# Kernel optimization log

Measured on AMD Instinct MI355X. Metric: run time of the kernel, lower is better.

Reference implementation:

```python
import jax, jax.numpy as jnp
import numpy as np
from jax import lax

B, CIN, COUT, H, W = 4, 256, 256, 64, 64
KH = KW = 3
STRIDE = PAD = DIL = 1
GROUPS = 1
K = KH * KW
HO = (H + 2 * PAD - DIL * (KH - 1) - 1) // STRIDE + 1
WO = (W + 2 * PAD - DIL * (KW - 1) - 1) // STRIDE + 1
DN = ('NCHW', 'OIHW', 'NCHW')


def _sep_conv(x, dw, pw):
    # Separable2d: depthwise kxk conv (stride/pad/dilation) then pointwise 1x1.
    y = lax.conv_general_dilated(x, dw, (STRIDE, STRIDE), [(PAD, PAD), (PAD, PAD)],
                                 rhs_dilation=(DIL, DIL), feature_group_count=x.shape[1],
                                 dimension_numbers=DN)
    return lax.conv_general_dilated(y, pw, (1, 1), 'VALID', dimension_numbers=DN)


def _deform_conv2d(x, offset, mask, weight, bias):
    Bb, Cin, Hh, Ww = x.shape
    O = weight.shape[0]
    G = offset.shape[1] // (2 * K)  # offset groups
    offs = offset.reshape(Bb, G, K, 2, HO, WO)
    dy, dx = offs[:, :, :, 0], offs[:, :, :, 1]  # [B,G,K,Ho,Wo]
    ki, kj = jnp.meshgrid(jnp.arange(KH), jnp.arange(KW), indexing='ij')
    base_y = (-PAD + ki.reshape(K, 1) * DIL + jnp.arange(HO)[None, :] * STRIDE).astype(x.dtype)  # [K,Ho]
    base_x = (-PAD + kj.reshape(K, 1) * DIL + jnp.arange(WO)[None, :] * STRIDE).astype(x.dtype)  # [K,Wo]
    py = base_y[None, None, :, :, None] + dy  # [B,G,K,Ho,Wo]
    px = base_x[None, None, :, None, :] + dx

    xg = x.reshape(Bb, G, Cin // G, Hh, Ww)

    def bilinear(img, py, px):
        # img [C,H,W], py/px [K,Ho,Wo]; zero-padding outside bounds.
        y0 = jnp.floor(py)
        x0 = jnp.floor(px)
        out = jnp.zeros((img.shape[0],) + py.shape, img.dtype)
        for a, (iy, wy) in enumerate((((y0), (y0 + 1 - py)), ((y0 + 1), (py - y0)))):
            for b, (ix, wx) in enumerate((((x0), (x0 + 1 - px)), ((x0 + 1), (px - x0)))):
                valid = (iy >= 0) & (iy < Hh) & (ix >= 0) & (ix < Ww)
                iyc = jnp.clip(iy, 0, Hh - 1).astype(jnp.int32)
                ixc = jnp.clip(ix, 0, Ww - 1).astype(jnp.int32)
                v = img[:, iyc, ixc]  # [C,K,Ho,Wo]
                out = out + v * (wy * wx * valid)[None]
        return out

    sampled = jax.vmap(jax.vmap(bilinear))(xg, py, px)  # [B,G,C/G,K,Ho,Wo]
    m = mask.reshape(Bb, G, K, HO, WO)
    sampled = sampled * m[:, :, None]

    cols = sampled.reshape(Bb, Cin, K, HO, WO).reshape(Bb, GROUPS, Cin // GROUPS, K, HO, WO)
    wr = weight.reshape(GROUPS, O // GROUPS, Cin // GROUPS, K)
    out = jnp.einsum('bgckhw,gock->bgohw', cols, wr).reshape(Bb, O, HO, WO)
    return out + bias[None, :, None, None]


def setup_inputs() -> dict:
    key = jax.random.key(0)
    ks = jax.random.split(key, 7)
    x = jax.random.normal(ks[0], (B, CIN, H, W), jnp.float32)
    weight = jax.random.normal(ks[1], (COUT, CIN // GROUPS, KH, KW), jnp.float32) / np.sqrt(CIN * K)
    bias = jax.random.normal(ks[2], (COUT,), jnp.float32) * 0.01
    off_dw = jax.random.normal(ks[3], (CIN, 1, KH, KW), jnp.float32) * 0.01
    off_pw = jax.random.normal(ks[4], (2 * K * GROUPS, CIN, 1, 1), jnp.float32) * 0.01
    mask_dw = jax.random.normal(ks[5], (CIN, 1, KH, KW), jnp.float32) * 0.01
    mask_pw = jax.random.normal(ks[6], (K * GROUPS, CIN, 1, 1), jnp.float32) * 0.01
    return dict(x=x, weight=weight, bias=bias, off_dw=off_dw, off_pw=off_pw,
                mask_dw=mask_dw, mask_pw=mask_pw)


def reference(x, weight, bias, off_dw, off_pw, mask_dw, mask_pw):
    offset = _sep_conv(x, off_dw, off_pw)                       # [B,2*K,Ho,Wo]
    mask = jax.nn.sigmoid(_sep_conv(x, mask_dw, mask_pw)) * 2.0  # MaskSigmoid(scale=2)
    return _deform_conv2d(x, offset, mask, weight, bias)
```

## Files before the change

### kernel.cpp

```cpp
#include <hip/hip_runtime.h>

#define CIN   256
#define COUT  256
#define HH    64
#define WW    64
#define KD    2304
#define NPIX  16384
#define SPLIT 16
#define CPS   (CIN / SPLIT)
#define NSTEP 18

typedef __attribute__((ext_vector_type(4))) float  float4v;
typedef __attribute__((ext_vector_type(4))) unsigned int uint4v;
typedef _Float16 h2 __attribute__((ext_vector_type(2)));
typedef _Float16 h8 __attribute__((ext_vector_type(8)));
typedef unsigned int u32;
typedef unsigned short u16;

__device__ __forceinline__ h2 as_h2(u32 v) { union { u32 u; h2 h; } x; x.u = v; return x.h; }
__device__ __forceinline__ u32 as_u32(h2 h) { union { u32 u; h2 h; } x; x.h = h; return x.u; }
__device__ __forceinline__ u16 f2h_bits(float f) { _Float16 h = (_Float16)f; return *(u16*)&h; }
__device__ __forceinline__ float h2f(u16 b) { _Float16 h = *(_Float16*)&b; return (float)h; }
__device__ __forceinline__ u32 packh2(float a, float b) {
  h2 h; h[0] = (_Float16)a; h[1] = (_Float16)b; return as_u32(h);
}

__device__ __forceinline__ void gload_lds16(const void* g, void* l) {
  __builtin_amdgcn_global_load_lds((const __attribute__((address_space(1))) u32*)g,
                                   (__attribute__((address_space(3))) u32*)l, 16, 0, 0);
}

__global__ __launch_bounds__(256) void offmask_part_kernel(
    const float* __restrict__ x,
    const float* __restrict__ off_dw, const float* __restrict__ off_pw,
    const float* __restrict__ mask_dw, const float* __restrict__ mask_pw,
    u32* __restrict__ part2)
{
  int m = blockIdx.x * 256 + threadIdx.x;
  int s = blockIdx.y;
  int b = m >> 12, pix = m & 4095;
  int ho = pix >> 6, wo = pix & 63;
  const float* xb = x + (size_t)b * CIN * 4096;

  float acc[27];
#pragma unroll
  for (int j = 0; j < 27; ++j) acc[j] = 0.f;

  int c0 = s * CPS;
  for (int ci = 0; ci < CPS; ++ci) {
    int c = c0 + ci;
    const float* xc = xb + (size_t)c * 4096;
    float d_off = 0.f, d_msk = 0.f;
#pragma unroll
    for (int t = 0; t < 9; ++t) {
      int gy = ho + t / 3 - 1, gx = wo + t % 3 - 1;
      bool ok = (gy >= 0) & (gy < HH) & (gx >= 0) & (gx < WW);
      float v = ok ? xc[gy * 64 + gx] : 0.f;
      d_off += v * off_dw[c * 9 + t];
      d_msk += v * mask_dw[c * 9 + t];
    }
#pragma unroll
    for (int j = 0; j < 18; ++j) acc[j] += d_off * off_pw[j * 256 + c];
#pragma unroll
    for (int j = 0; j < 9; ++j) acc[18 + j] += d_msk * mask_pw[j * 256 + c];
  }
  uint4v o[4];
#pragma unroll
  for (int k = 0; k < 13; ++k) o[k >> 2][k & 3] = packh2(acc[2 * k], acc[2 * k + 1]);
  o[3][1] = packh2(acc[26], 0.f);
  o[3][2] = 0; o[3][3] = 0;
  uint4v* pp = (uint4v*)(part2 + ((size_t)s * NPIX + m) * 16);
#pragma unroll
  for (int q = 0; q < 4; ++q) pp[q] = o[q];
}

__global__ __launch_bounds__(256) void offmask_reduce_kernel(
    const u32* __restrict__ part2, float* __restrict__ rec)
{
  int i = blockIdx.x * 256 + threadIdx.x;
  int m = i >> 4, k = i & 15;
  int j0 = 2 * k, j1 = 2 * k + 1;
  if (j0 >= 27) { rec[(size_t)m * 32 + j0] = 0.f; rec[(size_t)m * 32 + j1] = 0.f; return; }
  float s0 = 0.f, s1 = 0.f;
#pragma unroll
  for (int s = 0; s < SPLIT; ++s) {
    h2 v = as_h2(part2[((size_t)s * NPIX + m) * 16 + k]);
    s0 += (float)v[0]; s1 += (float)v[1];
  }
  rec[(size_t)m * 32 + j0] = (j0 < 18) ? s0 : 2.f / (1.f + __expf(-s0));
  rec[(size_t)m * 32 + j1] = (j1 < 18) ? s1 : ((j1 < 27) ? 2.f / (1.f + __expf(-s1)) : 0.f);
}

__global__ __launch_bounds__(256) void wconv_kernel(const float* __restrict__ w,
                                                    u16* __restrict__ wb)
{
  int i = blockIdx.x * 256 + threadIdx.x;
  int co = i / KD, rem = i - co * KD;
  int c = rem / 9, kk = rem - c * 9;
  wb[co * KD + kk * 256 + c] = f2h_bits(w[i]);
}

__global__ __launch_bounds__(256) void xpose_kernel(const float* __restrict__ x,
                                                    u16* __restrict__ xt)
{
  __shared__ float t[64][65];
  int ptile = blockIdx.x;
  int ctile = blockIdx.y;
  int b     = blockIdx.z;
  int tid = threadIdx.x;
  const float* xb = x + (size_t)b * CIN * 4096 + (size_t)ctile * 64 * 4096 + ptile * 64;
#pragma unroll
  for (int i = 0; i < 16; ++i) {
    int c = i * 4 + (tid >> 6), p = tid & 63;
    t[c][p] = xb[(size_t)c * 4096 + p];
  }
  __syncthreads();
  u16* xo = xt + ((size_t)b * 4096 + ptile * 64) * 256 + ctile * 64;
#pragma unroll
  for (int i = 0; i < 16; ++i) {
    int p = i * 4 + (tid >> 6), c = tid & 63;
    xo[(size_t)p * 256 + c] = f2h_bits(t[c][p]);
  }
}

__global__ __launch_bounds__(512, 2) void gemm_fused_kernel(
    const u16* __restrict__ A,
    const u16* __restrict__ xt,
    const float* __restrict__ rec,
    u16* __restrict__ tmp4)
{
  __shared__ __align__(16) u16 lA[3][256 * 32];
  __shared__ __align__(16) u16 lB[2][256 * 32];
  const int tid = threadIdx.x;
  const int ord = blockIdx.x;
  const int xcd = ord & 7, slot = ord >> 3;
  const int ptile = (slot >> 2) * 8 + xcd;
  const int h     = slot & 3;
  const int m0  = ptile * 256;
  const int b_img = ptile >> 4;
  const int cbase = h * 64;
  const int wave = tid >> 6, lane = tid & 63;
  const int wm = wave >> 1, wn = wave & 1;
  const int rl = lane & 15, kq = lane >> 4;
  const int sA = (kq ^ (rl & 3) ^ ((rl >> 2) & 3)) * 8;

  const int rA  = tid >> 2;
  const int koA = ((tid & 3) ^ (rA & 3) ^ ((rA >> 2) & 3)) * 8;
  const u16* aRow0 = A + (size_t)rA * KD + koA;
  const u16* aRow1 = A + (size_t)(rA + 128) * KD + koA;

  const int px_t = tid >> 1;
  const int chh  = (tid & 1) * 16;
  const int m_px = m0 + px_t;
  const int ho = (m_px & 4095) >> 6, wo = m_px & 63;
  const float* rp = rec + (size_t)m_px * 32;
  const u16* xb = xt + (size_t)b_img * 4096 * 256;
  const int swzp = (px_t & 3) ^ ((px_t >> 2) & 3);
  const int wAddr0 = px_t * 32 + ((((tid & 1) * 2)     ^ swzp) * 8);
  const int wAddr1 = px_t * 32 + ((((tid & 1) * 2 + 1) ^ swzp) * 8);

  u32 cOff[4];
  h2  wh[4];

#define KCOL(t_) (((t_) >> 1) * 256 + cbase + ((t_) & 1) * 32)

#define CALC_CORNERS(kk_) do {                                             \
    float dy = rp[(kk_) * 2], dx = rp[(kk_) * 2 + 1], msk = rp[18 + (kk_)];\
    float py  = (float)(ho - 1 + ((kk_) / 3)) + dy;                        \
    float pxf = (float)(wo - 1 + ((kk_) % 3)) + dx;                        \
    float fy = floorf(py), fx = floorf(pxf);                               \
    int y0 = (int)fy, x0 = (int)fx;                                        \
    float wy1 = py - fy, wy0 = 1.f - wy1;                                  \
    float wx1 = pxf - fx, wx0 = 1.f - wx1;                                 \
    _Pragma("unroll")                                                      \
    for (int cr = 0; cr < 4; ++cr) {                                       \
      int iy = y0 + (cr >> 1), ix = x0 + (cr & 1);                         \
      bool valid = (iy >= 0) & (iy < HH) & (ix >= 0) & (ix < WW);          \
      int iyc = min(max(iy, 0), HH - 1), ixc = min(max(ix, 0), WW - 1);    \
      cOff[cr] = (u32)(iyc * 64 + ixc) * 256;                              \
      float wy = (cr >> 1) ? wy1 : wy0;                                    \
      float wx = (cr & 1) ? wx1 : wx0;                                     \
      float wf = valid ? (wy * wx * msk) : 0.f;                            \
      _Float16 hw = (_Float16)wf;                                          \
      wh[cr] = (h2){hw, hw};                                               \
    }                                                                      \
  } while (0)

#define STAGE_A(k_, slot_) do {                                            \
    int k0_ = KCOL(k_);                                                    \
    gload_lds16(aRow0 + k0_, lA[slot_] + tid * 8);                         \
    gload_lds16(aRow1 + k0_, lA[slot_] + (tid + 512) * 8);                 \
  } while (0)

#define SAMP_LOAD(t_, va, vb) do {                                         \
    int c0n_ = cbase + ((t_) & 1) * 32 + chh;                              \
    _Pragma("unroll")                                                      \
    for (int cr = 0; cr < 4; ++cr) {                                       \
      va[cr] = *(const uint4v*)(xb + cOff[cr] + c0n_);                     \
      vb[cr] = *(const uint4v*)(xb + cOff[cr] + c0n_ + 8);                 \
    }                                                                      \
  } while (0)

#define BLEND_WRITE(bufi_, va, vb) do {                                    \
    uint4v o0, o1;                                                         \
    _Pragma("unroll")                                                      \
    for (int w_ = 0; w_ < 4; ++w_) {                                       \
      h2 s0_ = wh[0] * as_h2(va[0][w_]) + wh[1] * as_h2(va[1][w_]);        \
      s0_   += wh[2] * as_h2(va[2][w_]) + wh[3] * as_h2(va[3][w_]);        \
      h2 s1_ = wh[0] * as_h2(vb[0][w_]) + wh[1] * as_h2(vb[1][w_]);        \
      s1_   += wh[2] * as_h2(vb[2][w_]) + wh[3] * as_h2(vb[3][w_]);        \
      o0[w_] = as_u32(s0_); o1[w_] = as_u32(s1_);                          \
    }                                                                      \
    *(uint4v*)&lB[bufi_][wAddr0] = o0;                                     \
    *(uint4v*)&lB[bufi_][wAddr1] = o1;                                     \
  } while (0)

  float4v acc[4][8];
#pragma unroll
  for (int m = 0; m < 4; ++m)
#pragma unroll
    for (int n = 0; n < 8; ++n) acc[m][n] = float4v{0.f, 0.f, 0.f, 0.f};

  {
    CALC_CORNERS(0);
    uint4v va[4], vb[4];
    SAMP_LOAD(0, va, vb);
    STAGE_A(0, 0);
    STAGE_A(1, 1);
    asm volatile("s_waitcnt vmcnt(2)" ::: "memory");
    BLEND_WRITE(0, va, vb);
    asm volatile("s_waitcnt lgkmcnt(0)" ::: "memory");
    __builtin_amdgcn_s_barrier();
  }

  for (int it = 0; it < 3; ++it) {
#pragma unroll
    for (int u = 0; u < 6; ++u) {
      const int t = it * 6 + u;
      const int tn  = (t + 1 == NSTEP) ? 0 : t + 1;
      const int tn2 = (t + 2 >= NSTEP) ? (t + 2 - NSTEP) : t + 2;
      if ((tn & 1) == 0) CALC_CORNERS(tn >> 1);
      uint4v va[4], vb[4];
      SAMP_LOAD(tn, va, vb);
      STAGE_A(tn2, (u + 2) % 3);
      h8 af[4], bf[8];
#pragma unroll
      for (int m = 0; m < 4; ++m)
        af[m] = *(const h8*)&lA[u % 3][(wm * 64 + m * 16 + rl) * 32 + sA];
#pragma unroll
      for (int n = 0; n < 8; ++n)
        bf[n] = *(const h8*)&lB[u & 1][(wn * 128 + n * 16 + rl) * 32 + sA];
#pragma unroll
      for (int m = 0; m < 4; ++m)
#pragma unroll
        for (int n = 0; n < 8; ++n)
          acc[m][n] = __builtin_amdgcn_mfma_f32_16x16x32_f16(af[m], bf[n], acc[m][n], 0, 0, 0);
      asm volatile("s_waitcnt vmcnt(2)" ::: "memory");
      BLEND_WRITE((u + 1) & 1, va, vb);
      asm volatile("s_waitcnt lgkmcnt(0)" ::: "memory");
      __builtin_amdgcn_s_barrier();
    }
  }
#undef STAGE_A
#undef CALC_CORNERS
#undef SAMP_LOAD
#undef BLEND_WRITE
#undef KCOL

  const int p_base = (m0 & 4095) + wn * 128;
  u16* db = tmp4 + (size_t)h * COUT * NPIX + (size_t)b_img * COUT * 4096;
#pragma unroll
  for (int m = 0; m < 4; ++m) {
#pragma unroll
    for (int j = 0; j < 4; ++j) {
      int co = wm * 64 + m * 16 + kq * 4 + j;
#pragma unroll
      for (int n = 0; n < 8; ++n) {
        int pp = p_base + n * 16 + rl;
        db[(size_t)co * 4096 + pp] = f2h_bits(acc[m][n][j]);
      }
    }
  }
}

__global__ __launch_bounds__(256) void add_kernel(const u16* __restrict__ tmp4,
                                                  const float* __restrict__ bias,
                                                  float* __restrict__ out)
{
  size_t i = ((size_t)blockIdx.x * 256 + threadIdx.x) * 8;
  int co = (int)((i >> 12) & 255);
  float bv = bias[co];
  uint4v v0 = *(const uint4v*)(tmp4 + i);
  uint4v v1 = *(const uint4v*)(tmp4 + (size_t)COUT * NPIX + i);
  uint4v v2 = *(const uint4v*)(tmp4 + (size_t)2 * COUT * NPIX + i);
  uint4v v3 = *(const uint4v*)(tmp4 + (size_t)3 * COUT * NPIX + i);
  float4v oA, oB;
#pragma unroll
  for (int w = 0; w < 4; ++w) {
    h2 a = as_h2(v0[w]), b = as_h2(v1[w]), c = as_h2(v2[w]), d = as_h2(v3[w]);
    float lo = (float)a[0] + (float)b[0] + (float)c[0] + (float)d[0] + bv;
    float hi = (float)a[1] + (float)b[1] + (float)c[1] + (float)d[1] + bv;
    if (w < 2) { oA[w * 2] = lo; oA[w * 2 + 1] = hi; }
    else       { oB[(w - 2) * 2] = lo; oB[(w - 2) * 2 + 1] = hi; }
  }
  *(float4v*)(out + i) = oA;
  *(float4v*)(out + i + 4) = oB;
}

extern "C" void kernel_launch(void* const* d_in, const int* in_sizes, int n_in,
                              void* d_out, int out_size, void* d_ws, size_t ws_size,
                              hipStream_t stream) {
  const float* x       = (const float*)d_in[0];
  const float* weight  = (const float*)d_in[1];
  const float* bias    = (const float*)d_in[2];
  const float* off_dw  = (const float*)d_in[3];
  const float* off_pw  = (const float*)d_in[4];
  const float* mask_dw = (const float*)d_in[5];
  const float* mask_pw = (const float*)d_in[6];

  if (ws_size < 45219840ull) return;
  float* rec   = (float*)d_ws;
  u16*   wb    = (u16*)((char*)d_ws + 2097152);
  u16*   xt    = (u16*)((char*)d_ws + 3276800);
  u32*   part2 = (u32*)((char*)d_ws + 11665408);
  u16*   tmp4  = (u16*)((char*)d_ws + 11665408);
  float* out   = (float*)d_out;

  wconv_kernel<<<dim3(2304), dim3(256), 0, stream>>>(weight, wb);
  offmask_part_kernel<<<dim3(NPIX / 256, SPLIT), dim3(256), 0, stream>>>(
      x, off_dw, off_pw, mask_dw, mask_pw, part2);
  offmask_reduce_kernel<<<dim3(NPIX * 16 / 256), dim3(256), 0, stream>>>(part2, rec);
  xpose_kernel<<<dim3(64, 4, 4), dim3(256), 0, stream>>>(x, xt);
  gemm_fused_kernel<<<dim3(256), dim3(512), 0, stream>>>(wb, xt, rec, tmp4);
  add_kernel<<<dim3(COUT * NPIX / 8 / 256), dim3(256), 0, stream>>>(tmp4, bias, out);
}
```

Before: 92.89 us.

## Warp-specialize fused GEMM into producer and MFMA consumer waves with 2-way K split

Splits the 8 waves of the fused deformable GEMM into 4 producer waves, which do bilinear sampling into LDS and stage weights via global_load_lds, and 4 consumer waves that only issue MFMAs. The tile changes from 256 pixels with a 4-way channel split to 128 pixels with a 2-way split, so each block runs twice as many K steps. This halves the partial-sum scratch traffic and the work in the final add kernel. In exchange, only half the waves do MFMA work, each consumer wave holds a larger accumulator (8x4), and throughput depends on the producer keeping pace through barrier handshakes.

```diff
diff --git a/kernel.cpp b/kernel.cpp
--- a/kernel.cpp
+++ b/kernel.cpp
@@ -8,7 +8,7 @@
 #define NPIX  16384
 #define SPLIT 16
 #define CPS   (CIN / SPLIT)
-#define NSTEP 18
+#define NSTEP 36
 
 typedef __attribute__((ext_vector_type(4))) float  float4v;
 typedef __attribute__((ext_vector_type(4))) unsigned int uint4v;
@@ -20,7 +20,6 @@
 __device__ __forceinline__ h2 as_h2(u32 v) { union { u32 u; h2 h; } x; x.u = v; return x.h; }
 __device__ __forceinline__ u32 as_u32(h2 h) { union { u32 u; h2 h; } x; x.h = h; return x.u; }
 __device__ __forceinline__ u16 f2h_bits(float f) { _Float16 h = (_Float16)f; return *(u16*)&h; }
-__device__ __forceinline__ float h2f(u16 b) { _Float16 h = *(_Float16*)&b; return (float)h; }
 __device__ __forceinline__ u32 packh2(float a, float b) {
   h2 h; h[0] = (_Float16)a; h[1] = (_Float16)b; return as_u32(h);
 }
@@ -127,42 +126,45 @@
     const u16* __restrict__ A,
     const u16* __restrict__ xt,
     const float* __restrict__ rec,
-    u16* __restrict__ tmp4)
+    u16* __restrict__ tmp2)
 {
   __shared__ __align__(16) u16 lA[3][256 * 32];
-  __shared__ __align__(16) u16 lB[2][256 * 32];
+  __shared__ __align__(16) u16 lB[2][128 * 32];
   const int tid = threadIdx.x;
   const int ord = blockIdx.x;
   const int xcd = ord & 7, slot = ord >> 3;
-  const int ptile = (slot >> 2) * 8 + xcd;
-  const int h     = slot & 3;
-  const int m0  = ptile * 256;
-  const int b_img = ptile >> 4;
-  const int cbase = h * 64;
+  const int ptile = (slot >> 1) * 8 + xcd;
+  const int h     = slot & 1;
+  const int m0  = ptile * 128;
+  const int b_img = ptile >> 5;
+  const int cbase = h * 128;
   const int wave = tid >> 6, lane = tid & 63;
-  const int wm = wave >> 1, wn = wave & 1;
-  const int rl = lane & 15, kq = lane >> 4;
-  const int sA = (kq ^ (rl & 3) ^ ((rl >> 2) & 3)) * 8;
-
-  const int rA  = tid >> 2;
-  const int koA = ((tid & 3) ^ (rA & 3) ^ ((rA >> 2) & 3)) * 8;
-  const u16* aRow0 = A + (size_t)rA * KD + koA;
-  const u16* aRow1 = A + (size_t)(rA + 128) * KD + koA;
-
-  const int px_t = tid >> 1;
-  const int chh  = (tid & 1) * 16;
-  const int m_px = m0 + px_t;
-  const int ho = (m_px & 4095) >> 6, wo = m_px & 63;
-  const float* rp = rec + (size_t)m_px * 32;
-  const u16* xb = xt + (size_t)b_img * 4096 * 256;
-  const int swzp = (px_t & 3) ^ ((px_t >> 2) & 3);
-  const int wAddr0 = px_t * 32 + ((((tid & 1) * 2)     ^ swzp) * 8);
-  const int wAddr1 = px_t * 32 + ((((tid & 1) * 2 + 1) ^ swzp) * 8);
-
-  u32 cOff[4];
-  h2  wh[4];
-
-#define KCOL(t_) (((t_) >> 1) * 256 + cbase + ((t_) & 1) * 32)
+
+#define KCOL(t_) (((t_) >> 2) * 256 + cbase + ((t_) & 3) * 32)
+
+  if (wave < 4) {
+    const int p = tid;
+    u32 aDst[4]; const u16* aSrc[4];
+#pragma unroll
+    for (int q = 0; q < 4; ++q) {
+      int g = (wave * 4 + q) * 64 + lane;
+      int row = g >> 2, sub = g & 3;
+      int ko = (sub ^ (row & 3) ^ ((row >> 2) & 3)) * 8;
+      aSrc[q] = A + (size_t)row * KD + ko;
+      aDst[q] = g * 8;
+    }
+    const int px_t = p >> 1;
+    const int chh  = (p & 1) * 16;
+    const int m_px = m0 + px_t;
+    const int ho = (m_px & 4095) >> 6, wo = m_px & 63;
+    const float* rp = rec + (size_t)m_px * 32;
+    const u16* xb = xt + (size_t)b_img * 4096 * 256;
+    const int swzp = (px_t & 3) ^ ((px_t >> 2) & 3);
+    const int wAddr0 = px_t * 32 + ((((p & 1) * 2)     ^ swzp) * 8);
+    const int wAddr1 = px_t * 32 + ((((p & 1) * 2 + 1) ^ swzp) * 8);
+
+    u32 cOff[4];
+    h2  wh[4];
 
 #define CALC_CORNERS(kk_) do {                                             \
     float dy = rp[(kk_) * 2], dx = rp[(kk_) * 2 + 1], msk = rp[18 + (kk_)];\
@@ -186,14 +188,15 @@
     }                                                                      \
   } while (0)
 
-#define STAGE_A(k_, slot_) do {                                            \
+#define STAGE_A4(k_, slot_) do {                                           \
     int k0_ = KCOL(k_);                                                    \
-    gload_lds16(aRow0 + k0_, lA[slot_] + tid * 8);                         \
-    gload_lds16(aRow1 + k0_, lA[slot_] + (tid + 512) * 8);                 \
+    _Pragma("unroll")                                                      \
+    for (int q = 0; q < 4; ++q)                                            \
+      gload_lds16(aSrc[q] + k0_, lA[slot_] + aDst[q]);                     \
   } while (0)
 
 #define SAMP_LOAD(t_, va, vb) do {                                         \
-    int c0n_ = cbase + ((t_) & 1) * 32 + chh;                              \
+    int c0n_ = cbase + ((t_) & 3) * 32 + chh;                              \
     _Pragma("unroll")                                                      \
     for (int cr = 0; cr < 4; ++cr) {                                       \
       va[cr] = *(const uint4v*)(xb + cOff[cr] + c0n_);                     \
@@ -215,91 +218,103 @@
     *(uint4v*)&lB[bufi_][wAddr1] = o1;                                     \
   } while (0)
 
-  float4v acc[4][8];
-#pragma unroll
-  for (int m = 0; m < 4; ++m)
-#pragma unroll
-    for (int n = 0; n < 8; ++n) acc[m][n] = float4v{0.f, 0.f, 0.f, 0.f};
-
-  {
-    CALC_CORNERS(0);
-    uint4v va[4], vb[4];
-    SAMP_LOAD(0, va, vb);
-    STAGE_A(0, 0);
-    STAGE_A(1, 1);
-    asm volatile("s_waitcnt vmcnt(2)" ::: "memory");
-    BLEND_WRITE(0, va, vb);
-    asm volatile("s_waitcnt lgkmcnt(0)" ::: "memory");
-    __builtin_amdgcn_s_barrier();
-  }
-
-  for (int it = 0; it < 3; ++it) {
-#pragma unroll
-    for (int u = 0; u < 6; ++u) {
-      const int t = it * 6 + u;
-      const int tn  = (t + 1 == NSTEP) ? 0 : t + 1;
-      const int tn2 = (t + 2 >= NSTEP) ? (t + 2 - NSTEP) : t + 2;
-      if ((tn & 1) == 0) CALC_CORNERS(tn >> 1);
+    {
+      CALC_CORNERS(0);
       uint4v va[4], vb[4];
-      SAMP_LOAD(tn, va, vb);
-      STAGE_A(tn2, (u + 2) % 3);
-      h8 af[4], bf[8];
-#pragma unroll
-      for (int m = 0; m < 4; ++m)
-        af[m] = *(const h8*)&lA[u % 3][(wm * 64 + m * 16 + rl) * 32 + sA];
-#pragma unroll
-      for (int n = 0; n < 8; ++n)
-        bf[n] = *(const h8*)&lB[u & 1][(wn * 128 + n * 16 + rl) * 32 + sA];
-#pragma unroll
-      for (int m = 0; m < 4; ++m)
-#pragma unroll
-        for (int n = 0; n < 8; ++n)
-          acc[m][n] = __builtin_amdgcn_mfma_f32_16x16x32_f16(af[m], bf[n], acc[m][n], 0, 0, 0);
-      asm volatile("s_waitcnt vmcnt(2)" ::: "memory");
-      BLEND_WRITE((u + 1) & 1, va, vb);
+      SAMP_LOAD(0, va, vb);
+      STAGE_A4(0, 0);
+      STAGE_A4(1, 1);
+      asm volatile("s_waitcnt vmcnt(4)" ::: "memory");
+      BLEND_WRITE(0, va, vb);
       asm volatile("s_waitcnt lgkmcnt(0)" ::: "memory");
       __builtin_amdgcn_s_barrier();
     }
-  }
-#undef STAGE_A
+    for (int it = 0; it < 6; ++it) {
+#pragma unroll
+      for (int u = 0; u < 6; ++u) {
+        const int t = it * 6 + u;
+        const int tn  = (t + 1 == NSTEP) ? 0 : t + 1;
+        const int tn2 = (t + 2 >= NSTEP) ? (t + 2 - NSTEP) : t + 2;
+        if ((tn & 3) == 0) CALC_CORNERS(tn >> 2);
+        uint4v va[4], vb[4];
+        SAMP_LOAD(tn, va, vb);
+        STAGE_A4(tn2, (t + 2) % 3);
+        asm volatile("s_waitcnt vmcnt(4)" ::: "memory");
+        BLEND_WRITE((t + 1) & 1, va, vb);
+        asm volatile("s_waitcnt lgkmcnt(0)" ::: "memory");
+        __builtin_amdgcn_s_barrier();
+      }
+    }
 #undef CALC_CORNERS
+#undef STAGE_A4
 #undef SAMP_LOAD
 #undef BLEND_WRITE
+  } else {
+    const int cw = wave - 4;
+    const int wm = cw >> 1, wn = cw & 1;
+    const int rl = lane & 15, kq = lane >> 4;
+    const int sA = (kq ^ (rl & 3) ^ ((rl >> 2) & 3)) * 8;
+
+    float4v acc[8][4];
+#pragma unroll
+    for (int m = 0; m < 8; ++m)
+#pragma unroll
+      for (int n = 0; n < 4; ++n) acc[m][n] = float4v{0.f, 0.f, 0.f, 0.f};
+
+    __builtin_amdgcn_s_barrier();
+    for (int it = 0; it < 6; ++it) {
+#pragma unroll
+      for (int u = 0; u < 6; ++u) {
+        const int t = it * 6 + u;
+        h8 af[8], bf[4];
+#pragma unroll
+        for (int m = 0; m < 8; ++m)
+          af[m] = *(const h8*)&lA[t % 3][(wm * 128 + m * 16 + rl) * 32 + sA];
+#pragma unroll
+        for (int n = 0; n < 4; ++n)
+          bf[n] = *(const h8*)&lB[t & 1][(wn * 64 + n * 16 + rl) * 32 + sA];
+#pragma unroll
+        for (int m = 0; m < 8; ++m)
+#pragma unroll
+          for (int n = 0; n < 4; ++n)
+            acc[m][n] = __builtin_amdgcn_mfma_f32_16x16x32_f16(af[m], bf[n], acc[m][n], 0, 0, 0);
+        asm volatile("s_waitcnt lgkmcnt(0)" ::: "memory");
+        __builtin_amdgcn_s_barrier();
+      }
+    }
+    const int p_base = (m0 & 4095) + wn * 64;
+    u16* db = tmp2 + (size_t)h * COUT * NPIX + (size_t)b_img * COUT * 4096;
+#pragma unroll
+    for (int m = 0; m < 8; ++m) {
+#pragma unroll
+      for (int j = 0; j < 4; ++j) {
+        int co = wm * 128 + m * 16 + kq * 4 + j;
+#pragma unroll
+        for (int n = 0; n < 4; ++n) {
+          int pp = p_base + n * 16 + rl;
+          db[(size_t)co * 4096 + pp] = f2h_bits(acc[m][n][j]);
+        }
+      }
+    }
+  }
 #undef KCOL
-
-  const int p_base = (m0 & 4095) + wn * 128;
-  u16* db = tmp4 + (size_t)h * COUT * NPIX + (size_t)b_img * COUT * 4096;
-#pragma unroll
-  for (int m = 0; m < 4; ++m) {
-#pragma unroll
-    for (int j = 0; j < 4; ++j) {
-      int co = wm * 64 + m * 16 + kq * 4 + j;
-#pragma unroll
-      for (int n = 0; n < 8; ++n) {
-        int pp = p_base + n * 16 + rl;
-        db[(size_t)co * 4096 + pp] = f2h_bits(acc[m][n][j]);
-      }
-    }
-  }
-}
-
-__global__ __launch_bounds__(256) void add_kernel(const u16* __restrict__ tmp4,
+}
+
+__global__ __launch_bounds__(256) void add_kernel(const u16* __restrict__ tmp2,
                                                   const float* __restrict__ bias,
                                                   float* __restrict__ out)
 {
   size_t i = ((size_t)blockIdx.x * 256 + threadIdx.x) * 8;
   int co = (int)((i >> 12) & 255);
   float bv = bias[co];
-  uint4v v0 = *(const uint4v*)(tmp4 + i);
-  uint4v v1 = *(const uint4v*)(tmp4 + (size_t)COUT * NPIX + i);
-  uint4v v2 = *(const uint4v*)(tmp4 + (size_t)2 * COUT * NPIX + i);
-  uint4v v3 = *(const uint4v*)(tmp4 + (size_t)3 * COUT * NPIX + i);
+  uint4v v0 = *(const uint4v*)(tmp2 + i);
+  uint4v v1 = *(const uint4v*)(tmp2 + (size_t)COUT * NPIX + i);
   float4v oA, oB;
 #pragma unroll
   for (int w = 0; w < 4; ++w) {
-    h2 a = as_h2(v0[w]), b = as_h2(v1[w]), c = as_h2(v2[w]), d = as_h2(v3[w]);
-    float lo = (float)a[0] + (float)b[0] + (float)c[0] + (float)d[0] + bv;
-    float hi = (float)a[1] + (float)b[1] + (float)c[1] + (float)d[1] + bv;
+    h2 a = as_h2(v0[w]), b = as_h2(v1[w]);
+    float lo = (float)a[0] + (float)b[0] + bv;
+    float hi = (float)a[1] + (float)b[1] + bv;
     if (w < 2) { oA[w * 2] = lo; oA[w * 2 + 1] = hi; }
     else       { oB[(w - 2) * 2] = lo; oB[(w - 2) * 2 + 1] = hi; }
   }
@@ -318,12 +333,12 @@
   const float* mask_dw = (const float*)d_in[5];
   const float* mask_pw = (const float*)d_in[6];
 
-  if (ws_size < 45219840ull) return;
+  if (ws_size < 28442624ull) return;
   float* rec   = (float*)d_ws;
   u16*   wb    = (u16*)((char*)d_ws + 2097152);
   u16*   xt    = (u16*)((char*)d_ws + 3276800);
   u32*   part2 = (u32*)((char*)d_ws + 11665408);
-  u16*   tmp4  = (u16*)((char*)d_ws + 11665408);
+  u16*   tmp2  = (u16*)((char*)d_ws + 11665408);
   float* out   = (float*)d_out;
 
   wconv_kernel<<<dim3(2304), dim3(256), 0, stream>>>(weight, wb);
@@ -331,6 +346,6 @@
       x, off_dw, off_pw, mask_dw, mask_pw, part2);
   offmask_reduce_kernel<<<dim3(NPIX * 16 / 256), dim3(256), 0, stream>>>(part2, rec);
   xpose_kernel<<<dim3(64, 4, 4), dim3(256), 0, stream>>>(x, xt);
-  gemm_fused_kernel<<<dim3(256), dim3(512), 0, stream>>>(wb, xt, rec, tmp4);
-  add_kernel<<<dim3(COUT * NPIX / 8 / 256), dim3(256), 0, stream>>>(tmp4, bias, out);
-}
+  gemm_fused_kernel<<<dim3(256), dim3(512), 0, stream>>>(wb, xt, rec, tmp2);
+  add_kernel<<<dim3(COUT * NPIX / 8 / 256), dim3(256), 0, stream>>>(tmp2, bias, out);
+}
```

Measured after the change: 95.40 us. +2.7%, slower.

## Split GEMM K dimension eight ways to double grid size

Applied to the files above, without the earlier changes.

The fused deformable-sampling GEMM now splits the input channels into 8 slices of 32 instead of 4 slices of 64. This doubles the grid to 512 blocks, halves the per-block K loop to 9 steps, and raises the occupancy hint to 4 blocks per CU. The cost is eight fp16 partial outputs instead of four: more workspace, more partial-sum traffic in the add kernel, and bilinear corner math is now recomputed every step rather than every other step.

```diff
diff --git a/kernel.cpp b/kernel.cpp
--- a/kernel.cpp
+++ b/kernel.cpp
@@ -8,7 +8,7 @@
 #define NPIX  16384
 #define SPLIT 16
 #define CPS   (CIN / SPLIT)
-#define NSTEP 18
+#define NSTEP 9
 
 typedef __attribute__((ext_vector_type(4))) float  float4v;
 typedef __attribute__((ext_vector_type(4))) unsigned int uint4v;
@@ -20,7 +20,6 @@
 __device__ __forceinline__ h2 as_h2(u32 v) { union { u32 u; h2 h; } x; x.u = v; return x.h; }
 __device__ __forceinline__ u32 as_u32(h2 h) { union { u32 u; h2 h; } x; x.h = h; return x.u; }
 __device__ __forceinline__ u16 f2h_bits(float f) { _Float16 h = (_Float16)f; return *(u16*)&h; }
-__device__ __forceinline__ float h2f(u16 b) { _Float16 h = *(_Float16*)&b; return (float)h; }
 __device__ __forceinline__ u32 packh2(float a, float b) {
   h2 h; h[0] = (_Float16)a; h[1] = (_Float16)b; return as_u32(h);
 }
@@ -123,22 +122,22 @@
   }
 }
 
-__global__ __launch_bounds__(512, 2) void gemm_fused_kernel(
+__global__ __launch_bounds__(512, 4) void gemm_fused_kernel(
     const u16* __restrict__ A,
     const u16* __restrict__ xt,
     const float* __restrict__ rec,
-    u16* __restrict__ tmp4)
+    u16* __restrict__ tmp8)
 {
   __shared__ __align__(16) u16 lA[3][256 * 32];
   __shared__ __align__(16) u16 lB[2][256 * 32];
   const int tid = threadIdx.x;
   const int ord = blockIdx.x;
   const int xcd = ord & 7, slot = ord >> 3;
-  const int ptile = (slot >> 2) * 8 + xcd;
-  const int h     = slot & 3;
+  const int ptile = (slot >> 3) * 8 + xcd;
+  const int h     = slot & 7;
   const int m0  = ptile * 256;
   const int b_img = ptile >> 4;
-  const int cbase = h * 64;
+  const int cbase = h * 32;
   const int wave = tid >> 6, lane = tid & 63;
   const int wm = wave >> 1, wn = wave & 1;
   const int rl = lane & 15, kq = lane >> 4;
@@ -162,7 +161,7 @@
   u32 cOff[4];
   h2  wh[4];
 
-#define KCOL(t_) (((t_) >> 1) * 256 + cbase + ((t_) & 1) * 32)
+#define KCOL(t_) ((t_) * 256 + cbase)
 
 #define CALC_CORNERS(kk_) do {                                             \
     float dy = rp[(kk_) * 2], dx = rp[(kk_) * 2 + 1], msk = rp[18 + (kk_)];\
@@ -192,8 +191,8 @@
     gload_lds16(aRow1 + k0_, lA[slot_] + (tid + 512) * 8);                 \
   } while (0)
 
-#define SAMP_LOAD(t_, va, vb) do {                                         \
-    int c0n_ = cbase + ((t_) & 1) * 32 + chh;                              \
+#define SAMP_LOAD(va, vb) do {                                             \
+    int c0n_ = cbase + chh;                                                \
     _Pragma("unroll")                                                      \
     for (int cr = 0; cr < 4; ++cr) {                                       \
       va[cr] = *(const uint4v*)(xb + cOff[cr] + c0n_);                     \
@@ -224,7 +223,7 @@
   {
     CALC_CORNERS(0);
     uint4v va[4], vb[4];
-    SAMP_LOAD(0, va, vb);
+    SAMP_LOAD(va, vb);
     STAGE_A(0, 0);
     STAGE_A(1, 1);
     asm volatile("s_waitcnt vmcnt(2)" ::: "memory");
@@ -233,33 +232,30 @@
     __builtin_amdgcn_s_barrier();
   }
 
-  for (int it = 0; it < 3; ++it) {
-#pragma unroll
-    for (int u = 0; u < 6; ++u) {
-      const int t = it * 6 + u;
-      const int tn  = (t + 1 == NSTEP) ? 0 : t + 1;
-      const int tn2 = (t + 2 >= NSTEP) ? (t + 2 - NSTEP) : t + 2;
-      if ((tn & 1) == 0) CALC_CORNERS(tn >> 1);
-      uint4v va[4], vb[4];
-      SAMP_LOAD(tn, va, vb);
-      STAGE_A(tn2, (u + 2) % 3);
-      h8 af[4], bf[8];
-#pragma unroll
-      for (int m = 0; m < 4; ++m)
-        af[m] = *(const h8*)&lA[u % 3][(wm * 64 + m * 16 + rl) * 32 + sA];
+#pragma unroll
+  for (int t = 0; t < NSTEP; ++t) {
+    const int tn  = (t + 1 == NSTEP) ? 0 : t + 1;
+    const int tn2 = (t + 2 >= NSTEP) ? (t + 2 - NSTEP) : t + 2;
+    CALC_CORNERS(tn);
+    uint4v va[4], vb[4];
+    SAMP_LOAD(va, vb);
+    STAGE_A(tn2, (t + 2) % 3);
+    h8 af[4], bf[8];
+#pragma unroll
+    for (int m = 0; m < 4; ++m)
+      af[m] = *(const h8*)&lA[t % 3][(wm * 64 + m * 16 + rl) * 32 + sA];
+#pragma unroll
+    for (int n = 0; n < 8; ++n)
+      bf[n] = *(const h8*)&lB[t & 1][(wn * 128 + n * 16 + rl) * 32 + sA];
+#pragma unroll
+    for (int m = 0; m < 4; ++m)
 #pragma unroll
       for (int n = 0; n < 8; ++n)
-        bf[n] = *(const h8*)&lB[u & 1][(wn * 128 + n * 16 + rl) * 32 + sA];
-#pragma unroll
-      for (int m = 0; m < 4; ++m)
-#pragma unroll
-        for (int n = 0; n < 8; ++n)
-          acc[m][n] = __builtin_amdgcn_mfma_f32_16x16x32_f16(af[m], bf[n], acc[m][n], 0, 0, 0);
-      asm volatile("s_waitcnt vmcnt(2)" ::: "memory");
-      BLEND_WRITE((u + 1) & 1, va, vb);
-      asm volatile("s_waitcnt lgkmcnt(0)" ::: "memory");
-      __builtin_amdgcn_s_barrier();
-    }
+        acc[m][n] = __builtin_amdgcn_mfma_f32_16x16x32_f16(af[m], bf[n], acc[m][n], 0, 0, 0);
+    asm volatile("s_waitcnt vmcnt(2)" ::: "memory");
+    BLEND_WRITE((t + 1) & 1, va, vb);
+    asm volatile("s_waitcnt lgkmcnt(0)" ::: "memory");
+    __builtin_amdgcn_s_barrier();
   }
 #undef STAGE_A
 #undef CALC_CORNERS
@@ -268,7 +264,7 @@
 #undef KCOL
 
   const int p_base = (m0 & 4095) + wn * 128;
-  u16* db = tmp4 + (size_t)h * COUT * NPIX + (size_t)b_img * COUT * 4096;
+  u16* db = tmp8 + (size_t)h * COUT * NPIX + (size_t)b_img * COUT * 4096;
 #pragma unroll
   for (int m = 0; m < 4; ++m) {
 #pragma unroll
@@ -283,23 +279,26 @@
   }
 }
 
-__global__ __launch_bounds__(256) void add_kernel(const u16* __restrict__ tmp4,
+__global__ __launch_bounds__(256) void add_kernel(const u16* __restrict__ tmp8,
                                                   const float* __restrict__ bias,
                                                   float* __restrict__ out)
 {
   size_t i = ((size_t)blockIdx.x * 256 + threadIdx.x) * 8;
   int co = (int)((i >> 12) & 255);
   float bv = bias[co];
-  uint4v v0 = *(const uint4v*)(tmp4 + i);
-  uint4v v1 = *(const uint4v*)(tmp4 + (size_t)COUT * NPIX + i);
-  uint4v v2 = *(const uint4v*)(tmp4 + (size_t)2 * COUT * NPIX + i);
-  uint4v v3 = *(const uint4v*)(tmp4 + (size_t)3 * COUT * NPIX + i);
+  uint4v v[8];
+#pragma unroll
+  for (int s = 0; s < 8; ++s)
+    v[s] = *(const uint4v*)(tmp8 + (size_t)s * COUT * NPIX + i);
   float4v oA, oB;
 #pragma unroll
   for (int w = 0; w < 4; ++w) {
-    h2 a = as_h2(v0[w]), b = as_h2(v1[w]), c = as_h2(v2[w]), d = as_h2(v3[w]);
-    float lo = (float)a[0] + (float)b[0] + (float)c[0] + (float)d[0] + bv;
-    float hi = (float)a[1] + (float)b[1] + (float)c[1] + (float)d[1] + bv;
+    float lo = bv, hi = bv;
+#pragma unroll
+    for (int s = 0; s < 8; ++s) {
+      h2 a = as_h2(v[s][w]);
+      lo += (float)a[0]; hi += (float)a[1];
+    }
     if (w < 2) { oA[w * 2] = lo; oA[w * 2 + 1] = hi; }
     else       { oB[(w - 2) * 2] = lo; oB[(w - 2) * 2 + 1] = hi; }
   }
@@ -318,12 +317,12 @@
   const float* mask_dw = (const float*)d_in[5];
   const float* mask_pw = (const float*)d_in[6];
 
-  if (ws_size < 45219840ull) return;
+  if (ws_size < 78774272ull) return;
   float* rec   = (float*)d_ws;
   u16*   wb    = (u16*)((char*)d_ws + 2097152);
   u16*   xt    = (u16*)((char*)d_ws + 3276800);
   u32*   part2 = (u32*)((char*)d_ws + 11665408);
-  u16*   tmp4  = (u16*)((char*)d_ws + 11665408);
+  u16*   tmp8  = (u16*)((char*)d_ws + 11665408);
   float* out   = (float*)d_out;
 
   wconv_kernel<<<dim3(2304), dim3(256), 0, stream>>>(weight, wb);
@@ -331,6 +330,6 @@
       x, off_dw, off_pw, mask_dw, mask_pw, part2);
   offmask_reduce_kernel<<<dim3(NPIX * 16 / 256), dim3(256), 0, stream>>>(part2, rec);
   xpose_kernel<<<dim3(64, 4, 4), dim3(256), 0, stream>>>(x, xt);
-  gemm_fused_kernel<<<dim3(256), dim3(512), 0, stream>>>(wb, xt, rec, tmp4);
-  add_kernel<<<dim3(COUT * NPIX / 8 / 256), dim3(256), 0, stream>>>(tmp4, bias, out);
-}
+  gemm_fused_kernel<<<dim3(512), dim3(512), 0, stream>>>(wb, xt, rec, tmp8);
+  add_kernel<<<dim3(COUT * NPIX / 8 / 256), dim3(256), 0, stream>>>(tmp8, bias, out);
+}
```

Result: slower. 307.4 us (+231.0%).
